# Kernel tuning notes

Hardware: AMD Instinct MI355X
Metric: run time of the kernel (lower is better)

Reference implementation:

```python
import jax, jax.numpy as jnp
import numpy as np

EPS = 1e-8
TINY = 1e-12
C_L1 = float(np.sqrt(3.0 / (4.0 * np.pi)))  # integral-normalized l=1 SH coefficient


def _elu_feature_map(x):
    # positive_feature_map(kind='elu'): elu(x) + 1 > 0
    return jax.nn.elu(x) + 1.0


def _sph_bessel_j1(x):
    # j1(x) = sin(x)/x^2 - cos(x)/x, with series x/3 near 0 for stability
    small = x < 1e-4
    xs = jnp.where(small, 1.0, x)
    return jnp.where(small, x / 3.0, jnp.sin(xs) / (xs * xs) - jnp.cos(xs) / xs)


def setup_inputs() -> dict:
    key = jax.random.key(0)
    k1, k2, k3, k4, k5 = jax.random.split(key, 5)
    B, N, H, D, C, Q = 1, 2048, 8, 32, 32, 8
    pos = jax.random.normal(k1, (B, N, 3), dtype=jnp.float32) * 5.0
    q = jax.random.normal(k2, (B, N, H, D), dtype=jnp.float32)
    k = jax.random.normal(k3, (B, N, H, D), dtype=jnp.float32)
    v = jax.random.normal(k4, (B, N, H, C), dtype=jnp.float32)
    kappa = jnp.linspace(0.5, 4.0, Q, dtype=jnp.float32)          # (Q,) buffer
    a = jax.random.normal(k5, (H, Q), dtype=jnp.float32) * 0.1    # (H,Q) -> 'head' mode
    node_mask = jnp.ones((B, N), dtype=bool)
    return {"pos": pos, "q": q, "k": k, "v": v, "kappa": kappa, "a": a, "node_mask": node_mask}


def reference(pos, q, k, v, kappa, a, node_mask):
    B, N = pos.shape[0], pos.shape[1]
    m = node_mask.astype(pos.dtype)  # (B,N)

    # Linear (kernel) attention: alpha[b,h,i,j] = <phi(q_i), phi(k_j)> / sum_n <phi(q_i), phi(k_n)>
    phi_q = _elu_feature_map(q) * m[:, :, None, None]
    phi_k = _elu_feature_map(k) * m[:, :, None, None]
    v_m = v * m[:, :, None, None]
    logits = jnp.einsum('bihd,bjhd->bhij', phi_q, phi_k)
    denom = jnp.maximum(logits.sum(axis=-1, keepdims=True), EPS)
    alpha = logits / denom  # (B,H,N,N)

    # Pairwise geometry
    r_ij = pos[:, :, None, :] - pos[:, None, :, :]            # (B,N,N,3)
    dist = jnp.sqrt(jnp.sum(r_ij * r_ij, axis=-1) + TINY)     # (B,N,N)
    eye = jnp.eye(N, dtype=bool)
    safe_vec = jnp.array([1.0, 0.0, 0.0], dtype=pos.dtype)
    r_safe = jnp.where(eye[None, :, :, None], safe_vec, r_ij)

    # Real spherical harmonics, l=1, integral normalization, on normalized r_ij
    rn = jnp.sqrt(jnp.sum(r_safe * r_safe, axis=-1, keepdims=True) + TINY)
    Y = C_L1 * (r_safe / rn)  # (B,N,N,3) -> M=3 components

    # Radial part: f[b,h,i,j] = sum_q a[h,q] * j1(dist_ij * kappa_q)
    x = dist[..., None] * kappa  # (B,N,N,Q)
    jl = _sph_bessel_j1(x)
    f = jnp.einsum('bijq,hq->bhij', jl, a)

    # out[b,i,h,m,c] = sum_j alpha*f * Y * v
    w = alpha * f
    out = jnp.einsum('bhij,bijm,bjhc->bihmc', w, Y, v_m)
    return out  # (B, N, H, 2l+1=3, C)
```

## Files before the change

kernel.cpp:

```cpp
#include <hip/hip_runtime.h>

#define NN   2048
#define NH   8
#define ND   32
#define NC   32
#define NQ   8
#define JS   8
#define NOUT (NN*NH*3*NC)
#define EPSV 1e-8f
#define TINYV 1e-12f
#define C_L1 0.4886025119029199f
#define PSCALE 128.0f

typedef _Float16 half8 __attribute__((ext_vector_type(8)));
typedef __fp16   fp16x2 __attribute__((ext_vector_type(2)));
typedef float    f32x4 __attribute__((ext_vector_type(4)));
typedef float    f32x2 __attribute__((ext_vector_type(2)));

__device__ __forceinline__ float phi_elu(float x) { return x > 0.f ? x + 1.f : __expf(x); }
__device__ __forceinline__ float rfl(float x) {
    return __int_as_float(__builtin_amdgcn_readfirstlane(__float_as_int(x)));
}
__device__ __forceinline__ void glds16(const void* g, void* l) {
    __builtin_amdgcn_global_load_lds(
        (const __attribute__((address_space(1))) void*)g,
        (__attribute__((address_space(3))) void*)l, 16, 0, 0);
}

__global__ void k_prep(const float* __restrict__ pos, const float* __restrict__ q,
                       const float* __restrict__ k, const float* __restrict__ v,
                       const float* __restrict__ kappa, const float* __restrict__ a,
                       _Float16* __restrict__ phiQ16, _Float16* __restrict__ KtF,
                       _Float16* __restrict__ VtF, float* __restrict__ posT,
                       float* __restrict__ ksum, float* __restrict__ coef) {
    int b = blockIdx.x, t = threadIdx.x;
    if (b < 256) {
        int h = t >> 5, d = t & 31;
        int dg = d >> 3, e = d & 7;
        float ks = 0.f;
        for (int jj = 0; jj < 8; ++jj) {
            int j = b * 8 + jj;
            float pq = phi_elu(q[j * 256 + t]);
            float pk = phi_elu(k[j * 256 + t]);
            phiQ16[j * 256 + t] = (_Float16)pq;
            int jblk = j >> 5, jin = j & 31, jf = jin >> 4, lo = jin & 15;
            KtF[((((h * 64 + jblk) * 2 + jf) * 64) + dg * 16 + lo) * 8 + e] = (_Float16)pk;
            ks += pk;
        }
        atomicAdd(&ksum[t], ks);
    } else if (b < 512) {
        int unit = (b - 256) * 4 + (t >> 6);
        int lane = t & 63;
        int h = unit >> 7, jblk = (unit >> 1) & 63, cf = unit & 1;
        int hgrp = h >> 1, hh = h & 1;
        int c = cf * 16 + (lane & 15);
        int g8 = lane >> 4;
        half8 w0, w1, w2, w3;
        #pragma unroll
        for (int e = 0; e < 8; ++e) {
            int jl = g8 * 4 + (e & 3) + 16 * (e >> 2);
            int j = jblk * 32 + jl;
            float vv = v[(j * NH + h) * NC + c];
            w0[e] = (_Float16)vv;
            w1[e] = (_Float16)(vv * pos[j * 3 + 0]);
            w2[e] = (_Float16)(vv * pos[j * 3 + 1]);
            w3[e] = (_Float16)(vv * pos[j * 3 + 2]);
        }
        size_t fb = ((size_t)(jblk * 4 + hgrp) * 16 + hh * 2 + cf) * 64 + lane;
        ((half8*)VtF)[fb]        = w0;
        ((half8*)VtF)[fb + 256]  = w1;
        ((half8*)VtF)[fb + 512]  = w2;
        ((half8*)VtF)[fb + 768]  = w3;
    } else if (b < 536) {
        int idx = (b - 512) * 256 + t;
        if (idx < 3 * NN) {
            int comp = idx >> 11, j = idx & 2047;
            posT[comp * NN + j] = pos[j * 3 + comp];
        }
    } else {
        if (t < NH) {
            float An[8];
            #pragma unroll
            for (int n = 0; n < 8; ++n) An[n] = a[t * NQ + n];
            float k0 = kappa[0];
            float ik0 = 1.f / k0, ik02 = ik0 * ik0;
            const float Tc[9][9] = {
                {0,0,0,0,0,0,0,0,0},
                {0,1,0,0,0,0,0,0,0},
                {-1,0,2,0,0,0,0,0,0},
                {0,-3,0,4,0,0,0,0,0},
                {1,0,-8,0,8,0,0,0,0},
                {0,5,0,-20,0,16,0,0,0},
                {-1,0,18,0,-48,0,32,0,0},
                {0,-7,0,56,0,-112,0,64,0},
                {1,0,-32,0,160,0,-256,0,128}};
            const float Uc[9][8] = {
                {0,0,0,0,0,0,0,0},
                {1,0,0,0,0,0,0,0},
                {0,2,0,0,0,0,0,0},
                {-1,0,4,0,0,0,0,0},
                {0,-4,0,8,0,0,0,0},
                {1,0,-12,0,16,0,0,0},
                {0,6,0,-32,0,32,0,0},
                {-1,0,24,0,-80,0,64,0},
                {0,-8,0,80,0,-192,0,128}};
            #pragma unroll
            for (int kk = 0; kk < 9; ++kk) {
                float s = 0.f;
                #pragma unroll
                for (int n = 1; n <= 8; ++n) s = fmaf(An[n-1] * (1.f / n), Tc[n][kk], s);
                coef[kk * 8 + t] = s * ik0;
            }
            #pragma unroll
            for (int kk = 0; kk < 8; ++kk) {
                float s = 0.f;
                #pragma unroll
                for (int n = 1; n <= 8; ++n) s = fmaf(An[n-1] * (1.f / (n * n)), Uc[n][kk], s);
                coef[(9 + kk) * 8 + t] = s * ik02;
            }
        }
    }
}

__global__ void k_dinv(const _Float16* __restrict__ phiQ16, const float* __restrict__ ksum,
                       float* __restrict__ dinv) {
    int g = blockIdx.x * 256 + threadIdx.x;
    int h = g & 7;
    const half8* qv = (const half8*)phiQ16 + (size_t)g * 4;
    float s = 0.f;
    #pragma unroll
    for (int d4 = 0; d4 < 4; ++d4) {
        half8 x = qv[d4];
        #pragma unroll
        for (int e = 0; e < 8; ++e) s += (float)x[e] * ksum[h * 32 + d4 * 8 + e];
    }
    dinv[g] = C_L1 / fmaxf(s, EPSV);
}

__global__ __launch_bounds__(256, 3)
void k_main(const float* __restrict__ posT, const _Float16* __restrict__ phiQ16,
            const _Float16* __restrict__ KtF, const _Float16* __restrict__ VtF,
            const float* __restrict__ kappa, const float* __restrict__ coef,
            const float* __restrict__ dinvb, _Float16* __restrict__ part,
            float* __restrict__ out) {
    __shared__ __align__(16) char smem[2 * 16384];
    int tid = threadIdx.x;
    int wid = tid >> 6, lane = tid & 63;
    int li = lane & 15, g = lane >> 4;

    int bid = blockIdx.x;
    int hgrp = bid & 3, js = (bid >> 2) & 7, ib = bid >> 5;
    int itile = ib * 64 + wid * 16;

    float k0 = rfl(kappa[0]);

    float pc0[2];
    f32x2 cpq[2][8];
    #pragma unroll
    for (int hh = 0; hh < 2; ++hh) {
        int h = hgrp * 2 + hh;
        pc0[hh] = rfl(coef[h]);
        cpq[hh][0][0] = rfl(coef[8 * 8 + h]);
        cpq[hh][0][1] = rfl(coef[(9 + 7) * 8 + h]);
        #pragma unroll
        for (int kk = 1; kk <= 7; ++kk) {
            cpq[hh][kk][0] = rfl(coef[kk * 8 + h]);
            cpq[hh][kk][1] = rfl(coef[(9 + kk - 1) * 8 + h]);
        }
    }

    half8 qa[2];
    #pragma unroll
    for (int hh = 0; hh < 2; ++hh)
        qa[hh] = ((const half8*)phiQ16)[((size_t)(itile + li) * NH + hgrp * 2 + hh) * 4 + g];

    float pi0 = posT[itile + li];
    float pi1 = posT[NN + itile + li];
    float pi2 = posT[2 * NN + itile + li];

    f32x4 acc[2][4][2];
    #pragma unroll
    for (int hh = 0; hh < 2; ++hh)
      #pragma unroll
      for (int pl = 0; pl < 4; ++pl)
        #pragma unroll
        for (int cf = 0; cf < 2; ++cf)
          acc[hh][pl][cf] = (f32x4){0.f, 0.f, 0.f, 0.f};

    const int j0 = js * (NN / JS);
    const int NCHUNK = (NN / JS) / 32;
    const f32x4 z4 = (f32x4){0.f, 0.f, 0.f, 0.f};
    const int soff = wid * 4096 + lane * 16;

    {
        size_t sl = (size_t)((j0 >> 5) * 4 + hgrp);
        const char* src = (const char*)VtF + (sl << 14) + soff;
        char* dstl = smem + soff;
        #pragma unroll
        for (int kk = 0; kk < 4; ++kk)
            glds16(src + kk * 1024, dstl + kk * 1024);
    }

    #pragma unroll 1
    for (int t = 0; t < NCHUNK; ++t) {
        int jc = j0 + t * 32, jblk = jc >> 5;

        union { half8 h; fp16x2 p[4]; } wa[2];

        #pragma unroll
        for (int jF = 0; jF < 2; ++jF) {
            f32x4 pj4[3];
            #pragma unroll
            for (int m = 0; m < 3; ++m)
                pj4[m] = *(const f32x4*)(posT + m * NN + jc + jF * 16 + g * 4);

            f32x4 s[2];
            #pragma unroll
            for (int hh = 0; hh < 2; ++hh) {
                int h = hgrp * 2 + hh;
                half8 kf = ((const half8*)KtF)[((h * 64 + jblk) * 2 + jF) * 64 + lane];
                s[hh] = __builtin_amdgcn_mfma_f32_16x16x32_f16(kf, qa[hh], z4, 0, 0, 0);
            }

            float gux[2][4];
            #pragma unroll
            for (int r = 0; r < 4; ++r) {
                float dx = pi0 - pj4[0][r];
                float dy = pi1 - pj4[1][r];
                float dz = pi2 - pj4[2][r];
                float d2 = fmaf(dx, dx, fmaf(dy, dy, fmaf(dz, dz, TINYV)));
                float u = rsqrtf(d2);
                u = (d2 < 1e-10f) ? 0.f : u;
                float dist = d2 * u;
                float th = dist * k0;
                float sth, cth;
                __sincosf(th, &sth, &cth);
                float e1 = u * u;
                float ws = u * sth;
                f32x2 cc; cc[0] = cth; cc[1] = cth;
                #pragma unroll
                for (int hh = 0; hh < 2; ++hh) {
                    f32x2 pq = cpq[hh][0];
                    #pragma unroll
                    for (int kk = 7; kk >= 1; --kk)
                        pq = __builtin_elementwise_fma(pq, cc, cpq[hh][kk]);
                    float P = fmaf(pq[0], cth, pc0[hh]);
                    float inner = fmaf(ws, pq[1], -P);
                    gux[hh][r] = (s[hh][r] * e1) * inner;
                }
            }
            #pragma unroll
            for (int hh = 0; hh < 2; ++hh) {
                wa[hh].p[jF * 2 + 0] = __builtin_amdgcn_cvt_pkrtz(gux[hh][0], gux[hh][1]);
                wa[hh].p[jF * 2 + 1] = __builtin_amdgcn_cvt_pkrtz(gux[hh][2], gux[hh][3]);
            }
        }

        __syncthreads();

        const char* vb = smem + (t & 1) * 16384;
        #pragma unroll
        for (int hh = 0; hh < 2; ++hh) {
            #pragma unroll
            for (int pl = 0; pl < 4; ++pl) {
                half8 vf0 = *(const half8*)(vb + ((pl * 4 + hh * 2 + 0) * 1024) + lane * 16);
                half8 vf1 = *(const half8*)(vb + ((pl * 4 + hh * 2 + 1) * 1024) + lane * 16);
                acc[hh][pl][0] = __builtin_amdgcn_mfma_f32_16x16x32_f16(wa[hh].h, vf0, acc[hh][pl][0], 0, 0, 0);
                acc[hh][pl][1] = __builtin_amdgcn_mfma_f32_16x16x32_f16(wa[hh].h, vf1, acc[hh][pl][1], 0, 0, 0);
            }
        }

        if (t + 1 < NCHUNK) {
            size_t sl = (size_t)((jblk + 1) * 4 + hgrp);
            const char* src = (const char*)VtF + (sl << 14) + soff;
            char* dstl = smem + ((t + 1) & 1) * 16384 + soff;
            #pragma unroll
            for (int kk = 0; kk < 4; ++kk)
                glds16(src + kk * 1024, dstl + kk * 1024);
        }
    }

    f32x4 pi_ep[3];
    #pragma unroll
    for (int m = 0; m < 3; ++m)
        pi_ep[m] = *(const f32x4*)(posT + m * NN + itile + g * 4);

    bool last = (js == JS - 1);
    _Float16* pdst = part + (size_t)js * NOUT;
    #pragma unroll
    for (int hh = 0; hh < 2; ++hh) {
        int h = hgrp * 2 + hh;
        float dv[4];
        #pragma unroll
        for (int r = 0; r < 4; ++r) {
            dv[r] = dinvb[(itile + g * 4 + r) * NH + h];
            if (!last) dv[r] *= PSCALE;
        }
        #pragma unroll
        for (int m = 0; m < 3; ++m)
        #pragma unroll
        for (int cf = 0; cf < 2; ++cf)
        #pragma unroll
        for (int r = 0; r < 4; ++r) {
            int i = itile + g * 4 + r;
            size_t idx = ((size_t)i * NH + h) * 96 + m * 32 + cf * 16 + li;
            float val = fmaf(pi_ep[m][r], acc[hh][0][cf][r], -acc[hh][m + 1][cf][r]) * dv[r];
            if (last) out[idx] = val;
            else      pdst[idx] = (_Float16)val;
        }
    }
}

__global__ void k_reduce(const _Float16* __restrict__ part, float4* __restrict__ out) {
    int e = blockIdx.x * 256 + threadIdx.x;
    const int NO8 = NOUT / 8;
    if (e >= NO8) return;
    float4 o0 = out[e * 2], o1 = out[e * 2 + 1];
    const float S = 1.f / PSCALE;
    #pragma unroll
    for (int p = 0; p < JS - 1; ++p) {
        half8 t = ((const half8*)part)[(size_t)p * NO8 + e];
        o0.x = fmaf((float)t[0], S, o0.x);
        o0.y = fmaf((float)t[1], S, o0.y);
        o0.z = fmaf((float)t[2], S, o0.z);
        o0.w = fmaf((float)t[3], S, o0.w);
        o1.x = fmaf((float)t[4], S, o1.x);
        o1.y = fmaf((float)t[5], S, o1.y);
        o1.z = fmaf((float)t[6], S, o1.z);
        o1.w = fmaf((float)t[7], S, o1.w);
    }
    out[e * 2] = o0;
    out[e * 2 + 1] = o1;
}

extern "C" void kernel_launch(void* const* d_in, const int* in_sizes, int n_in,
                              void* d_out, int out_size, void* d_ws, size_t ws_size,
                              hipStream_t stream) {
    const float* pos   = (const float*)d_in[0];
    const float* q     = (const float*)d_in[1];
    const float* k     = (const float*)d_in[2];
    const float* v     = (const float*)d_in[3];
    const float* kappa = (const float*)d_in[4];
    const float* a     = (const float*)d_in[5];
    float* out = (float*)d_out;
    char* ws = (char*)d_ws;

    _Float16* phiQ16 = (_Float16*)(ws + 0);
    _Float16* KtF    = (_Float16*)(ws + (1u << 20));
    _Float16* VtF    = (_Float16*)(ws + (2u << 20));
    float*    posT   = (float*)   (ws + (6u << 20));
    float*    ksum   = (float*)   (ws + (6u << 20) + 24576);
    float*    dinvb  = (float*)   (ws + (6u << 20) + 25600);
    float*    coefb  = (float*)   (ws + (6u << 20) + 91136);
    _Float16* partb  = (_Float16*)(ws + (6u << 20) + 131072);

    (void)hipMemsetAsync(ksum, 0, 256 * sizeof(float), stream);
    k_prep<<<537, 256, 0, stream>>>(pos, q, k, v, kappa, a,
                                    phiQ16, KtF, VtF, posT, ksum, coefb);
    k_dinv<<<NN * NH / 256, 256, 0, stream>>>(phiQ16, ksum, dinvb);
    k_main<<<(NN / 64) * 4 * JS, 256, 0, stream>>>(posT, phiQ16, KtF, VtF,
                                                   kappa, coefb, dinvb, partb, out);
    k_reduce<<<(NOUT / 8 + 255) / 256, 256, 0, stream>>>(partb, (float4*)out);
}
```

Baseline: 70.07 us.

## Fuse denominator computation into main kernel and prefetch K fragments

Drops the separate k_dinv launch and computes the normalization denominator in the k_main epilogue from the resident Q fragments and ksum, combined with wave shuffles. Every j-split now writes fp16 partials, so the reduce kernel no longer reads a float out buffer written by the last split. K fragments for the next chunk are register-prefetched alongside the V LDS prefetch, which is issued earlier, before the MFMA accumulation. This removes one kernel launch and dependency and hides K load latency, at the cost of extra registers and an fp16 rounding of the last split's partial.

```diff
diff --git a/kernel.cpp b/kernel.cpp
--- a/kernel.cpp
+++ b/kernel.cpp
@@ -122,27 +122,11 @@
     }
 }
 
-__global__ void k_dinv(const _Float16* __restrict__ phiQ16, const float* __restrict__ ksum,
-                       float* __restrict__ dinv) {
-    int g = blockIdx.x * 256 + threadIdx.x;
-    int h = g & 7;
-    const half8* qv = (const half8*)phiQ16 + (size_t)g * 4;
-    float s = 0.f;
-    #pragma unroll
-    for (int d4 = 0; d4 < 4; ++d4) {
-        half8 x = qv[d4];
-        #pragma unroll
-        for (int e = 0; e < 8; ++e) s += (float)x[e] * ksum[h * 32 + d4 * 8 + e];
-    }
-    dinv[g] = C_L1 / fmaxf(s, EPSV);
-}
-
 __global__ __launch_bounds__(256, 3)
 void k_main(const float* __restrict__ posT, const _Float16* __restrict__ phiQ16,
             const _Float16* __restrict__ KtF, const _Float16* __restrict__ VtF,
             const float* __restrict__ kappa, const float* __restrict__ coef,
-            const float* __restrict__ dinvb, _Float16* __restrict__ part,
-            float* __restrict__ out) {
+            const float* __restrict__ ksum, _Float16* __restrict__ part) {
     __shared__ __align__(16) char smem[2 * 16384];
     int tid = threadIdx.x;
     int wid = tid >> 6, lane = tid & 63;
@@ -192,8 +176,16 @@
     const f32x4 z4 = (f32x4){0.f, 0.f, 0.f, 0.f};
     const int soff = wid * 4096 + lane * 16;
 
+    half8 kf[2][2], kfn[2][2];
     {
-        size_t sl = (size_t)((j0 >> 5) * 4 + hgrp);
+        int jblk0 = j0 >> 5;
+        #pragma unroll
+        for (int hh = 0; hh < 2; ++hh)
+            #pragma unroll
+            for (int jF = 0; jF < 2; ++jF)
+                kf[hh][jF] = ((const half8*)KtF)[
+                    (((hgrp * 2 + hh) * 64 + jblk0) * 2 + jF) * 64 + lane];
+        size_t sl = (size_t)(jblk0 * 4 + hgrp);
         const char* src = (const char*)VtF + (sl << 14) + soff;
         char* dstl = smem + soff;
         #pragma unroll
@@ -216,11 +208,8 @@
 
             f32x4 s[2];
             #pragma unroll
-            for (int hh = 0; hh < 2; ++hh) {
-                int h = hgrp * 2 + hh;
-                half8 kf = ((const half8*)KtF)[((h * 64 + jblk) * 2 + jF) * 64 + lane];
-                s[hh] = __builtin_amdgcn_mfma_f32_16x16x32_f16(kf, qa[hh], z4, 0, 0, 0);
-            }
+            for (int hh = 0; hh < 2; ++hh)
+                s[hh] = __builtin_amdgcn_mfma_f32_16x16x32_f16(kf[hh][jF], qa[hh], z4, 0, 0, 0);
 
             float gux[2][4];
             #pragma unroll
@@ -258,6 +247,22 @@
 
         __syncthreads();
 
+        if (t + 1 < NCHUNK) {
+            int jn = jblk + 1;
+            #pragma unroll
+            for (int hh = 0; hh < 2; ++hh)
+                #pragma unroll
+                for (int jF = 0; jF < 2; ++jF)
+                    kfn[hh][jF] = ((const half8*)KtF)[
+                        (((hgrp * 2 + hh) * 64 + jn) * 2 + jF) * 64 + lane];
+            size_t sl = (size_t)(jn * 4 + hgrp);
+            const char* src = (const char*)VtF + (sl << 14) + soff;
+            char* dstl = smem + ((t + 1) & 1) * 16384 + soff;
+            #pragma unroll
+            for (int kk = 0; kk < 4; ++kk)
+                glds16(src + kk * 1024, dstl + kk * 1024);
+        }
+
         const char* vb = smem + (t & 1) * 16384;
         #pragma unroll
         for (int hh = 0; hh < 2; ++hh) {
@@ -271,12 +276,11 @@
         }
 
         if (t + 1 < NCHUNK) {
-            size_t sl = (size_t)((jblk + 1) * 4 + hgrp);
-            const char* src = (const char*)VtF + (sl << 14) + soff;
-            char* dstl = smem + ((t + 1) & 1) * 16384 + soff;
-            #pragma unroll
-            for (int kk = 0; kk < 4; ++kk)
-                glds16(src + kk * 1024, dstl + kk * 1024);
+            #pragma unroll
+            for (int hh = 0; hh < 2; ++hh)
+                #pragma unroll
+                for (int jF = 0; jF < 2; ++jF)
+                    kf[hh][jF] = kfn[hh][jF];
         }
     }
 
@@ -285,17 +289,25 @@
     for (int m = 0; m < 3; ++m)
         pi_ep[m] = *(const f32x4*)(posT + m * NN + itile + g * 4);
 
-    bool last = (js == JS - 1);
-    _Float16* pdst = part + (size_t)js * NOUT;
+    float dinvC[2][4];
     #pragma unroll
     for (int hh = 0; hh < 2; ++hh) {
         int h = hgrp * 2 + hh;
-        float dv[4];
-        #pragma unroll
-        for (int r = 0; r < 4; ++r) {
-            dv[r] = dinvb[(itile + g * 4 + r) * NH + h];
-            if (!last) dv[r] *= PSCALE;
-        }
+        float p = 0.f;
+        #pragma unroll
+        for (int e = 0; e < 8; ++e) p += (float)qa[hh][e] * ksum[h * 32 + g * 8 + e];
+        p += __shfl_xor(p, 16);
+        p += __shfl_xor(p, 32);
+        float dcol = (C_L1 * PSCALE) / fmaxf(p, EPSV);
+        #pragma unroll
+        for (int r = 0; r < 4; ++r)
+            dinvC[hh][r] = __shfl(dcol, g * 4 + r);
+    }
+
+    _Float16* pdst = part + (size_t)js * NOUT;
+    #pragma unroll
+    for (int hh = 0; hh < 2; ++hh) {
+        int h = hgrp * 2 + hh;
         #pragma unroll
         for (int m = 0; m < 3; ++m)
         #pragma unroll
@@ -304,9 +316,8 @@
         for (int r = 0; r < 4; ++r) {
             int i = itile + g * 4 + r;
             size_t idx = ((size_t)i * NH + h) * 96 + m * 32 + cf * 16 + li;
-            float val = fmaf(pi_ep[m][r], acc[hh][0][cf][r], -acc[hh][m + 1][cf][r]) * dv[r];
-            if (last) out[idx] = val;
-            else      pdst[idx] = (_Float16)val;
+            float val = fmaf(pi_ep[m][r], acc[hh][0][cf][r], -acc[hh][m + 1][cf][r]);
+            pdst[idx] = (_Float16)(val * dinvC[hh][r]);
         }
     }
 }
@@ -315,22 +326,16 @@
     int e = blockIdx.x * 256 + threadIdx.x;
     const int NO8 = NOUT / 8;
     if (e >= NO8) return;
-    float4 o0 = out[e * 2], o1 = out[e * 2 + 1];
+    float s[8] = {0.f, 0.f, 0.f, 0.f, 0.f, 0.f, 0.f, 0.f};
+    #pragma unroll
+    for (int p = 0; p < JS; ++p) {
+        half8 t = ((const half8*)part)[(size_t)p * NO8 + e];
+        #pragma unroll
+        for (int x = 0; x < 8; ++x) s[x] += (float)t[x];
+    }
     const float S = 1.f / PSCALE;
-    #pragma unroll
-    for (int p = 0; p < JS - 1; ++p) {
-        half8 t = ((const half8*)part)[(size_t)p * NO8 + e];
-        o0.x = fmaf((float)t[0], S, o0.x);
-        o0.y = fmaf((float)t[1], S, o0.y);
-        o0.z = fmaf((float)t[2], S, o0.z);
-        o0.w = fmaf((float)t[3], S, o0.w);
-        o1.x = fmaf((float)t[4], S, o1.x);
-        o1.y = fmaf((float)t[5], S, o1.y);
-        o1.z = fmaf((float)t[6], S, o1.z);
-        o1.w = fmaf((float)t[7], S, o1.w);
-    }
-    out[e * 2] = o0;
-    out[e * 2 + 1] = o1;
+    out[e * 2]     = make_float4(s[0] * S, s[1] * S, s[2] * S, s[3] * S);
+    out[e * 2 + 1] = make_float4(s[4] * S, s[5] * S, s[6] * S, s[7] * S);
 }
 
 extern "C" void kernel_launch(void* const* d_in, const int* in_sizes, int n_in,
@@ -350,15 +355,13 @@
     _Float16* VtF    = (_Float16*)(ws + (2u << 20));
     float*    posT   = (float*)   (ws + (6u << 20));
     float*    ksum   = (float*)   (ws + (6u << 20) + 24576);
-    float*    dinvb  = (float*)   (ws + (6u << 20) + 25600);
     float*    coefb  = (float*)   (ws + (6u << 20) + 91136);
     _Float16* partb  = (_Float16*)(ws + (6u << 20) + 131072);
 
     (void)hipMemsetAsync(ksum, 0, 256 * sizeof(float), stream);
     k_prep<<<537, 256, 0, stream>>>(pos, q, k, v, kappa, a,
                                     phiQ16, KtF, VtF, posT, ksum, coefb);
-    k_dinv<<<NN * NH / 256, 256, 0, stream>>>(phiQ16, ksum, dinvb);
     k_main<<<(NN / 64) * 4 * JS, 256, 0, stream>>>(posT, phiQ16, KtF, VtF,
-                                                   kappa, coefb, dinvb, partb, out);
+                                                   kappa, coefb, ksum, partb);
     k_reduce<<<(NOUT / 8 + 255) / 256, 256, 0, stream>>>(partb, (float4*)out);
 }
```

New measurement: 68.74 us. No clear change (-1.9%).
